# Kernel optimization log

Hardware: AMD Instinct MI355X
Metric: run time of the kernel (lower is better)

The kernel has to match this reference:

```python
import jax, jax.numpy as jnp
import numpy as np

B, S, H, HKV, D = 2, 1024, 32, 8, 128


def _rope_tables(seq_len, head_dim, base=10000.0):
    inv_freq = 1.0 / (base ** (np.arange(0, head_dim, 2, dtype=np.float32) / head_dim))
    freqs = np.arange(seq_len, dtype=np.float32)[:, None] * inv_freq[None, :]  # [S, D/2]
    emb = np.concatenate([freqs, freqs], axis=-1)  # [S, D] (Llama layout)
    return jnp.asarray(np.cos(emb)), jnp.asarray(np.sin(emb))


def setup_inputs() -> dict:
    key = jax.random.key(0)
    kq, kk, kv = jax.random.split(key, 3)
    q = jax.random.normal(kq, (B, S, H, D), dtype=jnp.float32)
    k = jax.random.normal(kk, (B, S, HKV, D), dtype=jnp.float32)
    v = jax.random.normal(kv, (B, S, HKV, D), dtype=jnp.float32)
    cos, sin = _rope_tables(S, D)
    # additive causal mask [B, 1, S, S]: 0 where allowed, large negative where masked
    causal = jnp.tril(jnp.ones((S, S), dtype=bool))
    mask = jnp.where(causal, 0.0, -1e9).astype(jnp.float32)
    attention_mask = jnp.broadcast_to(mask[None, None], (B, 1, S, S))
    softmax_scale = 1.0 / float(np.sqrt(D))
    return {
        "query_states": q, "key_states": k, "value_states": v,
        "cos": cos, "sin": sin, "attention_mask": attention_mask,
        "softmax_scale": softmax_scale,
    }


def _apply_rope(x, cos, sin):
    # x: [B, S, h, D]; cos/sin: [S, D]
    d2 = x.shape[-1] // 2
    rot = jnp.concatenate([-x[..., d2:], x[..., :d2]], axis=-1)  # rotate_half
    return x * cos[None, :, None, :] + rot * sin[None, :, None, :]


def reference(query_states, key_states, value_states, cos, sin, attention_mask, softmax_scale):
    b, s, h, d = query_states.shape
    hkv = key_states.shape[2]
    g = h // hkv  # GQA group size
    q = _apply_rope(query_states, cos, sin)
    k = _apply_rope(key_states, cos, sin)
    qg = q.reshape(b, s, hkv, g, d)
    # scores: [B, Hkv, G, Q, K]
    scores = jnp.einsum('bqhgd,bkhd->bhgqk', qg, k) * softmax_scale
    scores = scores + attention_mask[:, :, None]  # [B,1,Q,K] -> broadcast over (Hkv, G)
    p = jax.nn.softmax(scores, axis=-1)
    out = jnp.einsum('bhgqk,bkhd->bqhgd', p, value_states)
    return out.reshape(b, s, h, d)
```

## Files before the change

kernel.cpp:

```cpp
#include <hip/hip_runtime.h>

#define S_LEN 1024
#define D_DIM 128
#define NH    32
#define NKV   8
#define NB    2

typedef __bf16 bf16x8 __attribute__((ext_vector_type(8)));
typedef float  f32x4  __attribute__((ext_vector_type(4)));
typedef unsigned short u16x8 __attribute__((ext_vector_type(8)));

__device__ __forceinline__ unsigned short f2bf(float f) {
    unsigned int u = __float_as_uint(f);
    u += 0x7fffu + ((u >> 16) & 1u);
    return (unsigned short)(u >> 16);
}

__device__ __forceinline__ void gld_lds16(const unsigned short* g, unsigned short* l) {
    __builtin_amdgcn_global_load_lds(
        (const __attribute__((address_space(1))) unsigned int*)(g),
        (__attribute__((address_space(3))) unsigned int*)(l), 16, 0, 0);
}

__global__ __launch_bounds__(256) void rope_q_kernel(
    const float* __restrict__ q, const float* __restrict__ cosb,
    const float* __restrict__ sinb, const float* __restrict__ scale_ptr,
    unsigned short* __restrict__ Qr)
{
    const float sc = *scale_ptr * 1.44269504088896f;
    int gid = blockIdx.x * 256 + threadIdx.x;
    int row = gid >> 6;
    int j   = gid & 63;
    int h  = row & (NH - 1);
    int bs = row >> 5;
    int s  = bs & (S_LEN - 1);
    int b  = bs >> 10;
    const float* qp = q + (size_t)row * D_DIM;
    float x0 = qp[j];
    float x1 = qp[j + 64];
    float c  = cosb[s * D_DIM + j];
    float sn = sinb[s * D_DIM + j];
    size_t orow = ((size_t)(b * NH + h) * S_LEN + s) * D_DIM;
    Qr[orow + j]      = f2bf((x0 * c - x1 * sn) * sc);
    Qr[orow + j + 64] = f2bf((x1 * c + x0 * sn) * sc);
}

__global__ __launch_bounds__(256) void rope_k_kernel(
    const float* __restrict__ k, const float* __restrict__ cosb,
    const float* __restrict__ sinb, unsigned short* __restrict__ Kr)
{
    int gid = blockIdx.x * 256 + threadIdx.x;
    int row = gid >> 6;
    int j   = gid & 63;
    int hk = row & (NKV - 1);
    int bs = row >> 3;
    int s  = bs & (S_LEN - 1);
    int b  = bs >> 10;
    const float* kp = k + (size_t)row * D_DIM;
    float x0 = kp[j];
    float x1 = kp[j + 64];
    float c  = cosb[s * D_DIM + j];
    float sn = sinb[s * D_DIM + j];
    size_t orow = ((size_t)(b * NKV + hk) * S_LEN + s) * D_DIM;
    Kr[orow + j]      = f2bf(x0 * c - x1 * sn);
    Kr[orow + j + 64] = f2bf(x1 * c + x0 * sn);
}

__global__ __launch_bounds__(256) void transpose_v_kernel(
    const float* __restrict__ v, unsigned short* __restrict__ Vt)
{
    int blk   = blockIdx.x;
    int stile = blk & 15;
    int hk    = (blk >> 4) & (NKV - 1);
    int b     = blk >> 7;
    int tid   = threadIdx.x;
    __shared__ unsigned short tile[64][132];
#pragma unroll
    for (int i = 0; i < 8; i++) {
        int e    = i * 256 + tid;
        int srow = e >> 5;
        int dq   = (e & 31) * 4;
        const float* vp = v + (((size_t)(b * S_LEN + stile * 64 + srow) * NKV + hk) * D_DIM + dq);
        float4 val = *(const float4*)vp;
        tile[srow][dq + 0] = f2bf(val.x);
        tile[srow][dq + 1] = f2bf(val.y);
        tile[srow][dq + 2] = f2bf(val.z);
        tile[srow][dq + 3] = f2bf(val.w);
    }
    __syncthreads();
    size_t head = (size_t)(b * NKV + hk) * D_DIM * S_LEN;
#pragma unroll
    for (int i = 0; i < 4; i++) {
        int g  = i * 256 + tid;
        int d  = g >> 3;
        int c8 = g & 7;
        int s0 = c8 * 8;
        u16x8 pk;
#pragma unroll
        for (int jj = 0; jj < 8; jj++) pk[jj] = tile[s0 + jj][d];
        *(u16x8*)(Vt + head + (size_t)d * S_LEN + stile * 64 + s0) = pk;
    }
}

__global__ __launch_bounds__(256, 2) void attn_kernel(
    const unsigned short* __restrict__ Qr,
    const unsigned short* __restrict__ Kr,
    const unsigned short* __restrict__ Vt,
    float* __restrict__ out)
{
    const int p    = blockIdx.x;
    const int h    = blockIdx.y;
    const int b    = blockIdx.z;
    const int hk   = h >> 2;
    const int tid  = threadIdx.x;
    const int w    = tid >> 6;
    const int lane = tid & 63;
    const int lr   = lane & 15;
    const int lg   = lane >> 4;

    __shared__ unsigned short Kt[2][64 * 128];
    __shared__ unsigned short Vs[2][128 * 64];
    __shared__ unsigned short Pb[4][16 * 64];

    const unsigned short* khead = Kr + (size_t)(b * NKV + hk) * S_LEN * D_DIM;
    const unsigned short* vhead = Vt + (size_t)(b * NKV + hk) * D_DIM * S_LEN;

    auto stage = [&](int u, int buf) {
        const unsigned short* kt = khead + (size_t)u * 64 * D_DIM;
#pragma unroll
        for (int n = 0; n < 4; n++) {
            int row = w * 16 + n * 4 + (lane >> 4);
            int cc  = (lane & 15) ^ (row & 7);
            gld_lds16(kt + (size_t)row * D_DIM + cc * 8,
                      &Kt[buf][(w * 16 + n * 4) * 128]);
        }
        const unsigned short* vt = vhead + u * 64;
#pragma unroll
        for (int n = 0; n < 4; n++) {
            int d  = w * 32 + n * 8 + (lane >> 3);
            int cc = (lane & 7) ^ (d & 7);
            gld_lds16(vt + (size_t)d * S_LEN + cc * 8,
                      &Vs[buf][(w * 32 + n * 8) * 64]);
        }
    };

#pragma unroll 1
    for (int pass = 0; pass < 2; ++pass) {
        const int qt = (pass == 0) ? (15 - p) : p;

        const unsigned short* qbase =
            Qr + ((size_t)(b * NH + h) * S_LEN + qt * 64 + w * 16 + lr) * D_DIM;
        bf16x8 qf[4];
#pragma unroll
        for (int kk = 0; kk < 4; kk++)
            qf[kk] = *(const bf16x8*)(qbase + lg * 8 + kk * 32);

        f32x4 o[8];
#pragma unroll
        for (int dt = 0; dt < 8; dt++) o[dt] = f32x4{0.f, 0.f, 0.f, 0.f};
        float m_run = -1e30f, lsum = 0.f;

        if (pass) __syncthreads();
        stage(0, 0);

#pragma unroll 1
        for (int u = 0; u <= qt; ++u) {
            const int cur = u & 1;
            __syncthreads();
            if (u < qt) stage(u + 1, cur ^ 1);

            f32x4 st[4];
#pragma unroll
            for (int kj = 0; kj < 4; kj++) st[kj] = f32x4{0.f, 0.f, 0.f, 0.f};
            __builtin_amdgcn_s_setprio(1);
#pragma unroll
            for (int kj = 0; kj < 4; kj++) {
                if (u < qt || kj <= w) {
                    int row = kj * 16 + lr;
#pragma unroll
                    for (int kk = 0; kk < 4; kk++) {
                        int cs = (lg + kk * 4) ^ (row & 7);
                        bf16x8 kf = *(const bf16x8*)(&Kt[cur][row * 128 + cs * 8]);
                        st[kj] = __builtin_amdgcn_mfma_f32_16x16x32_bf16(kf, qf[kk], st[kj], 0, 0, 0);
                    }
                }
            }
            __builtin_amdgcn_s_setprio(0);

            if (u == qt) {
#pragma unroll
                for (int kj = 0; kj < 4; kj++)
#pragma unroll
                    for (int r = 0; r < 4; r++)
                        if (kj * 16 + lg * 4 + r > w * 16 + lr) st[kj][r] = -1e30f;
            }

            float lmax = fmaxf(fmaxf(fmaxf(st[0][0], st[0][1]), fmaxf(st[0][2], st[0][3])),
                               fmaxf(fmaxf(st[1][0], st[1][1]), fmaxf(st[1][2], st[1][3])));
            lmax = fmaxf(lmax,
                   fmaxf(fmaxf(fmaxf(st[2][0], st[2][1]), fmaxf(st[2][2], st[2][3])),
                         fmaxf(fmaxf(st[3][0], st[3][1]), fmaxf(st[3][2], st[3][3]))));
            float pm = fmaxf(lmax, __shfl_xor(lmax, 16));
            pm = fmaxf(pm, __shfl_xor(pm, 32));

            if (__any(pm > m_run + 8.f)) {
                float mnew = fmaxf(m_run, pm);
                float ps   = exp2f(m_run - mnew);
                m_run = mnew;
                lsum *= ps;
#pragma unroll
                for (int r = 0; r < 4; r++) {
                    float psr = __shfl(ps, lg * 4 + r);
#pragma unroll
                    for (int dt = 0; dt < 8; dt++) o[dt][r] *= psr;
                }
            }
            float lsloc = 0.f;
#pragma unroll
            for (int kj = 0; kj < 4; kj++)
#pragma unroll
                for (int r = 0; r < 4; r++) {
                    float pv = exp2f(st[kj][r] - m_run);
                    st[kj][r] = pv;
                    lsloc += pv;
                }
            float t = lsloc + __shfl_xor(lsloc, 16);
            t += __shfl_xor(t, 32);
            lsum += t;

            char* pw = (char*)&Pb[w][0];
#pragma unroll
            for (int kj = 0; kj < 4; kj++) {
                unsigned int w0 = (unsigned)f2bf(st[kj][0]) | ((unsigned)f2bf(st[kj][1]) << 16);
                unsigned int w1 = (unsigned)f2bf(st[kj][2]) | ((unsigned)f2bf(st[kj][3]) << 16);
                int C = (2 * kj + (lg >> 1)) ^ (lr & 7);
                *(uint2*)(pw + lr * 128 + C * 16 + (lg & 1) * 8) = uint2{w0, w1};
            }

            __builtin_amdgcn_s_setprio(1);
#pragma unroll
            for (int kk2 = 0; kk2 < 2; kk2++) {
                int Cp = (lg + 4 * kk2) ^ (lr & 7);
                bf16x8 pf = *(const bf16x8*)(pw + lr * 128 + Cp * 16);
#pragma unroll
                for (int dt = 0; dt < 8; dt++) {
                    int vrow = dt * 16 + lr;
                    int cs = (lg + kk2 * 4) ^ (vrow & 7);
                    bf16x8 vf = *(const bf16x8*)(&Vs[cur][vrow * 64 + cs * 8]);
                    o[dt] = __builtin_amdgcn_mfma_f32_16x16x32_bf16(pf, vf, o[dt], 0, 0, 0);
                }
            }
            __builtin_amdgcn_s_setprio(0);
        }

        float rcp = 1.0f / lsum;
        float invr[4];
#pragma unroll
        for (int r = 0; r < 4; r++) invr[r] = __shfl(rcp, lg * 4 + r);
        float* obase = out + ((size_t)(b * S_LEN + qt * 64 + w * 16) * NH + h) * D_DIM;
#pragma unroll
        for (int dt = 0; dt < 8; dt++)
#pragma unroll
            for (int r = 0; r < 4; r++)
                obase[(size_t)(lg * 4 + r) * NH * D_DIM + dt * 16 + lr] = o[dt][r] * invr[r];
    }
}

extern "C" void kernel_launch(void* const* d_in, const int* in_sizes, int n_in,
                              void* d_out, int out_size, void* d_ws, size_t ws_size,
                              hipStream_t stream) {
    const float* q    = (const float*)d_in[0];
    const float* k    = (const float*)d_in[1];
    const float* v    = (const float*)d_in[2];
    const float* cosb = (const float*)d_in[3];
    const float* sinb = (const float*)d_in[4];
    const float* scale = (const float*)d_in[6];
    float* out = (float*)d_out;

    unsigned short* Qr = (unsigned short*)d_ws;
    unsigned short* Kr = Qr + (size_t)NB * NH  * S_LEN * D_DIM;
    unsigned short* Vt = Kr + (size_t)NB * NKV * S_LEN * D_DIM;

    rope_q_kernel<<<NB * S_LEN * NH / 4, 256, 0, stream>>>(q, cosb, sinb, scale, Qr);
    rope_k_kernel<<<NB * S_LEN * NKV / 4, 256, 0, stream>>>(k, cosb, sinb, Kr);
    transpose_v_kernel<<<NB * NKV * (S_LEN / 64), 256, 0, stream>>>(v, Vt);
    dim3 grid(8, NH, NB);
    attn_kernel<<<grid, 256, 0, stream>>>(Qr, Kr, Vt, out);
}
```

Baseline: 66.26 us.

## Switch attention to 32x32x16 MFMA with 512-thread blocks over 256-query tiles

Rewrites the attention kernel to use 32x32x16 bf16 MFMA instructions, with each of 8 waves owning 32 query rows in a 256-row tile. The P matrix stays in registers as the A operand instead of round-tripping through LDS. The paired-tile causal balancing is replaced by a swizzled 1-D grid of 256 blocks. Each K/V tile staged in LDS now serves 256 query rows, which cuts redundant loads, but the causal work is unevenly spread across blocks and waves that sit idle on masked tiles still wait at the barriers.

```diff
diff --git a/kernel.cpp b/kernel.cpp
--- a/kernel.cpp
+++ b/kernel.cpp
@@ -7,8 +7,9 @@
 #define NB    2
 
 typedef __bf16 bf16x8 __attribute__((ext_vector_type(8)));
-typedef float  f32x4  __attribute__((ext_vector_type(4)));
+typedef float  f32x16 __attribute__((ext_vector_type(16)));
 typedef unsigned short u16x8 __attribute__((ext_vector_type(8)));
+typedef unsigned int   u32x4 __attribute__((ext_vector_type(4)));
 
 __device__ __forceinline__ unsigned short f2bf(float f) {
     unsigned int u = __float_as_uint(f);
@@ -74,7 +75,7 @@
     int hk    = (blk >> 4) & (NKV - 1);
     int b     = blk >> 7;
     int tid   = threadIdx.x;
-    __shared__ unsigned short tile[64][132];
+    __shared__ __align__(16) unsigned short tile[64][132];
 #pragma unroll
     for (int i = 0; i < 8; i++) {
         int e    = i * 256 + tid;
@@ -102,106 +103,118 @@
     }
 }
 
-__global__ __launch_bounds__(256, 2) void attn_kernel(
+__global__ __launch_bounds__(512, 2) void attn_kernel(
     const unsigned short* __restrict__ Qr,
     const unsigned short* __restrict__ Kr,
     const unsigned short* __restrict__ Vt,
     float* __restrict__ out)
 {
-    const int p    = blockIdx.x;
-    const int h    = blockIdx.y;
-    const int b    = blockIdx.z;
-    const int hk   = h >> 2;
+    const int bid = blockIdx.x;
+    const int swz = (bid & 7) * 32 + (bid >> 3);
+    const int t  = swz & 3;
+    const int h  = (swz >> 2) & 31;
+    const int b  = swz >> 7;
+    const int hk = h >> 2;
+
     const int tid  = threadIdx.x;
     const int w    = tid >> 6;
     const int lane = tid & 63;
-    const int lr   = lane & 15;
-    const int lg   = lane >> 4;
-
-    __shared__ unsigned short Kt[2][64 * 128];
-    __shared__ unsigned short Vs[2][128 * 64];
-    __shared__ unsigned short Pb[4][16 * 64];
+    const int ln   = lane & 31;
+    const int hi   = lane >> 5;
+
+    __shared__ __align__(16) unsigned short Kt[2][64 * 128];
+    __shared__ __align__(16) unsigned short Vs[2][128 * 64];
+
+    const int q0 = t * 256 + w * 32;
+    const int qg = q0 + ln;
 
     const unsigned short* khead = Kr + (size_t)(b * NKV + hk) * S_LEN * D_DIM;
     const unsigned short* vhead = Vt + (size_t)(b * NKV + hk) * D_DIM * S_LEN;
 
+    const int krow = lane >> 4;
+    const int kcc  = lane & 15;
+    const int vrw  = lane >> 3;
+    const int vcc  = lane & 7;
+
     auto stage = [&](int u, int buf) {
         const unsigned short* kt = khead + (size_t)u * 64 * D_DIM;
 #pragma unroll
-        for (int n = 0; n < 4; n++) {
-            int row = w * 16 + n * 4 + (lane >> 4);
-            int cc  = (lane & 15) ^ (row & 7);
-            gld_lds16(kt + (size_t)row * D_DIM + cc * 8,
-                      &Kt[buf][(w * 16 + n * 4) * 128]);
+        for (int n = 0; n < 2; n++) {
+            int row = w * 8 + n * 4 + krow;
+            int cc  = kcc ^ (row & 7);
+            gld_lds16(kt + (size_t)row * D_DIM + cc * 8, &Kt[buf][(w * 8 + n * 4) * 128]);
         }
-        const unsigned short* vt = vhead + u * 64;
-#pragma unroll
-        for (int n = 0; n < 4; n++) {
-            int d  = w * 32 + n * 8 + (lane >> 3);
-            int cc = (lane & 7) ^ (d & 7);
-            gld_lds16(vt + (size_t)d * S_LEN + cc * 8,
-                      &Vs[buf][(w * 32 + n * 8) * 64]);
+        const unsigned short* vt = vhead + (size_t)u * 64;
+#pragma unroll
+        for (int n = 0; n < 2; n++) {
+            int d  = w * 16 + n * 8 + vrw;
+            int cc = vcc ^ (d & 7);
+            gld_lds16(vt + (size_t)d * S_LEN + cc * 8, &Vs[buf][(w * 16 + n * 8) * 64]);
         }
     };
 
+    const unsigned short* qrow =
+        Qr + ((size_t)(b * NH + h) * S_LEN + qg) * D_DIM + hi * 8;
+    bf16x8 qf[8];
+#pragma unroll
+    for (int dd = 0; dd < 8; dd++)
+        qf[dd] = *(const bf16x8*)(qrow + dd * 16);
+
+    f32x16 o[4];
+#pragma unroll
+    for (int dt = 0; dt < 4; dt++)
+#pragma unroll
+        for (int r = 0; r < 16; r++) o[dt][r] = 0.f;
+    float m_run = -1e30f, lsum = 0.f;
+
+    const int U = 4 * t + 4;
+    stage(0, 0);
+
 #pragma unroll 1
-    for (int pass = 0; pass < 2; ++pass) {
-        const int qt = (pass == 0) ? (15 - p) : p;
-
-        const unsigned short* qbase =
-            Qr + ((size_t)(b * NH + h) * S_LEN + qt * 64 + w * 16 + lr) * D_DIM;
-        bf16x8 qf[4];
-#pragma unroll
-        for (int kk = 0; kk < 4; kk++)
-            qf[kk] = *(const bf16x8*)(qbase + lg * 8 + kk * 32);
-
-        f32x4 o[8];
-#pragma unroll
-        for (int dt = 0; dt < 8; dt++) o[dt] = f32x4{0.f, 0.f, 0.f, 0.f};
-        float m_run = -1e30f, lsum = 0.f;
-
-        if (pass) __syncthreads();
-        stage(0, 0);
-
-#pragma unroll 1
-        for (int u = 0; u <= qt; ++u) {
-            const int cur = u & 1;
-            __syncthreads();
-            if (u < qt) stage(u + 1, cur ^ 1);
-
-            f32x4 st[4];
-#pragma unroll
-            for (int kj = 0; kj < 4; kj++) st[kj] = f32x4{0.f, 0.f, 0.f, 0.f};
+    for (int u = 0; u < U; ++u) {
+        const int cur = u & 1;
+        __syncthreads();
+        if (u + 1 < U) stage(u + 1, cur ^ 1);
+
+        if (64 * u <= q0 + 31) {
+            const bool act1 = (64 * u + 32 <= q0 + 31);
+
+            f32x16 st[2];
+#pragma unroll
+            for (int r = 0; r < 16; r++) { st[0][r] = 0.f; st[1][r] = 0.f; }
             __builtin_amdgcn_s_setprio(1);
 #pragma unroll
-            for (int kj = 0; kj < 4; kj++) {
-                if (u < qt || kj <= w) {
-                    int row = kj * 16 + lr;
-#pragma unroll
-                    for (int kk = 0; kk < 4; kk++) {
-                        int cs = (lg + kk * 4) ^ (row & 7);
-                        bf16x8 kf = *(const bf16x8*)(&Kt[cur][row * 128 + cs * 8]);
-                        st[kj] = __builtin_amdgcn_mfma_f32_16x16x32_bf16(kf, qf[kk], st[kj], 0, 0, 0);
+            for (int s = 0; s < 2; s++) {
+                if (s == 0 || act1) {
+#pragma unroll
+                    for (int dd = 0; dd < 8; dd++) {
+                        int row = s * 32 + ln;
+                        int c   = (2 * dd + hi) ^ (row & 7);
+                        bf16x8 kf = *(const bf16x8*)(&Kt[cur][row * 128 + c * 8]);
+                        st[s] = __builtin_amdgcn_mfma_f32_32x32x16_bf16(kf, qf[dd], st[s], 0, 0, 0);
                     }
                 }
             }
             __builtin_amdgcn_s_setprio(0);
 
-            if (u == qt) {
-#pragma unroll
-                for (int kj = 0; kj < 4; kj++)
-#pragma unroll
-                    for (int r = 0; r < 4; r++)
-                        if (kj * 16 + lg * 4 + r > w * 16 + lr) st[kj][r] = -1e30f;
-            }
-
-            float lmax = fmaxf(fmaxf(fmaxf(st[0][0], st[0][1]), fmaxf(st[0][2], st[0][3])),
-                               fmaxf(fmaxf(st[1][0], st[1][1]), fmaxf(st[1][2], st[1][3])));
-            lmax = fmaxf(lmax,
-                   fmaxf(fmaxf(fmaxf(st[2][0], st[2][1]), fmaxf(st[2][2], st[2][3])),
-                         fmaxf(fmaxf(st[3][0], st[3][1]), fmaxf(st[3][2], st[3][3]))));
-            float pm = fmaxf(lmax, __shfl_xor(lmax, 16));
-            pm = fmaxf(pm, __shfl_xor(pm, 32));
+            if (64 * u + 63 > q0) {
+#pragma unroll
+                for (int s = 0; s < 2; s++)
+#pragma unroll
+                    for (int r = 0; r < 16; r++) {
+                        int kg = 64 * u + 32 * s + (r & 3) + 8 * (r >> 2) + 4 * hi;
+                        if (kg > qg) st[s][r] = -1e30f;
+                    }
+            }
+
+            float mx = -1e30f;
+#pragma unroll
+            for (int r = 0; r < 16; r++) mx = fmaxf(mx, st[0][r]);
+            if (act1) {
+#pragma unroll
+                for (int r = 0; r < 16; r++) mx = fmaxf(mx, st[1][r]);
+            }
+            float pm = fmaxf(mx, __shfl_xor(mx, 32));
 
             if (__any(pm > m_run + 8.f)) {
                 float mnew = fmaxf(m_run, pm);
@@ -209,60 +222,66 @@
                 m_run = mnew;
                 lsum *= ps;
 #pragma unroll
-                for (int r = 0; r < 4; r++) {
-                    float psr = __shfl(ps, lg * 4 + r);
-#pragma unroll
-                    for (int dt = 0; dt < 8; dt++) o[dt][r] *= psr;
+                for (int r = 0; r < 16; r++) {
+                    float psr = __shfl(ps, (r & 3) + 8 * (r >> 2) + 4 * hi);
+#pragma unroll
+                    for (int dt = 0; dt < 4; dt++) o[dt][r] *= psr;
                 }
             }
-            float lsloc = 0.f;
-#pragma unroll
-            for (int kj = 0; kj < 4; kj++)
-#pragma unroll
-                for (int r = 0; r < 4; r++) {
-                    float pv = exp2f(st[kj][r] - m_run);
-                    st[kj][r] = pv;
-                    lsloc += pv;
+            float ls = 0.f;
+#pragma unroll
+            for (int r = 0; r < 16; r++) {
+                float p = exp2f(st[0][r] - m_run);
+                st[0][r] = p; ls += p;
+            }
+            if (act1) {
+#pragma unroll
+                for (int r = 0; r < 16; r++) {
+                    float p = exp2f(st[1][r] - m_run);
+                    st[1][r] = p; ls += p;
                 }
-            float t = lsloc + __shfl_xor(lsloc, 16);
-            t += __shfl_xor(t, 32);
-            lsum += t;
-
-            char* pw = (char*)&Pb[w][0];
-#pragma unroll
-            for (int kj = 0; kj < 4; kj++) {
-                unsigned int w0 = (unsigned)f2bf(st[kj][0]) | ((unsigned)f2bf(st[kj][1]) << 16);
-                unsigned int w1 = (unsigned)f2bf(st[kj][2]) | ((unsigned)f2bf(st[kj][3]) << 16);
-                int C = (2 * kj + (lg >> 1)) ^ (lr & 7);
-                *(uint2*)(pw + lr * 128 + C * 16 + (lg & 1) * 8) = uint2{w0, w1};
-            }
-
+            }
+            lsum += ls + __shfl_xor(ls, 32);
+
+            const char* vbase = (const char*)&Vs[cur][0];
             __builtin_amdgcn_s_setprio(1);
 #pragma unroll
-            for (int kk2 = 0; kk2 < 2; kk2++) {
-                int Cp = (lg + 4 * kk2) ^ (lr & 7);
-                bf16x8 pf = *(const bf16x8*)(pw + lr * 128 + Cp * 16);
-#pragma unroll
-                for (int dt = 0; dt < 8; dt++) {
-                    int vrow = dt * 16 + lr;
-                    int cs = (lg + kk2 * 4) ^ (vrow & 7);
-                    bf16x8 vf = *(const bf16x8*)(&Vs[cur][vrow * 64 + cs * 8]);
-                    o[dt] = __builtin_amdgcn_mfma_f32_16x16x32_bf16(pf, vf, o[dt], 0, 0, 0);
+            for (int ks = 0; ks < 4; ks++) {
+                if (ks < 2 || act1) {
+                    const f32x16& sv = st[ks >> 1];
+                    const int g = (ks & 1) * 8;
+                    unsigned int d0 = (unsigned)f2bf(sv[g + 0]) | ((unsigned)f2bf(sv[g + 1]) << 16);
+                    unsigned int d1 = (unsigned)f2bf(sv[g + 2]) | ((unsigned)f2bf(sv[g + 3]) << 16);
+                    unsigned int d2 = (unsigned)f2bf(sv[g + 4]) | ((unsigned)f2bf(sv[g + 5]) << 16);
+                    unsigned int d3 = (unsigned)f2bf(sv[g + 6]) | ((unsigned)f2bf(sv[g + 7]) << 16);
+                    u32x4 paw = {d0, d1, d2, d3};
+                    bf16x8 pa = __builtin_bit_cast(bf16x8, paw);
+#pragma unroll
+                    for (int dt = 0; dt < 4; dt++) {
+                        int d = dt * 32 + ln;
+                        const char* vrow = vbase + d * 128;
+                        int x = d & 7;
+                        uint2 vlo = *(const uint2*)(vrow + (((2 * ks)     ^ x) * 16) + hi * 8);
+                        uint2 vhi = *(const uint2*)(vrow + (((2 * ks + 1) ^ x) * 16) + hi * 8);
+                        u32x4 vw = {vlo.x, vlo.y, vhi.x, vhi.y};
+                        bf16x8 vf = __builtin_bit_cast(bf16x8, vw);
+                        o[dt] = __builtin_amdgcn_mfma_f32_32x32x16_bf16(pa, vf, o[dt], 0, 0, 0);
+                    }
                 }
             }
             __builtin_amdgcn_s_setprio(0);
         }
-
-        float rcp = 1.0f / lsum;
-        float invr[4];
-#pragma unroll
-        for (int r = 0; r < 4; r++) invr[r] = __shfl(rcp, lg * 4 + r);
-        float* obase = out + ((size_t)(b * S_LEN + qt * 64 + w * 16) * NH + h) * D_DIM;
-#pragma unroll
-        for (int dt = 0; dt < 8; dt++)
-#pragma unroll
-            for (int r = 0; r < 4; r++)
-                obase[(size_t)(lg * 4 + r) * NH * D_DIM + dt * 16 + lr] = o[dt][r] * invr[r];
+    }
+
+    float rcp = 1.0f / lsum;
+    float* ob = out + ((size_t)(b * S_LEN + q0) * NH + h) * D_DIM;
+#pragma unroll
+    for (int r = 0; r < 16; r++) {
+        int qo = (r & 3) + 8 * (r >> 2) + 4 * hi;
+        float invr = __shfl(rcp, qo);
+#pragma unroll
+        for (int dt = 0; dt < 4; dt++)
+            ob[(size_t)qo * NH * D_DIM + dt * 32 + ln] = o[dt][r] * invr;
     }
 }
 
@@ -284,6 +303,5 @@
     rope_q_kernel<<<NB * S_LEN * NH / 4, 256, 0, stream>>>(q, cosb, sinb, scale, Qr);
     rope_k_kernel<<<NB * S_LEN * NKV / 4, 256, 0, stream>>>(k, cosb, sinb, Kr);
     transpose_v_kernel<<<NB * NKV * (S_LEN / 64), 256, 0, stream>>>(v, Vt);
-    dim3 grid(8, NH, NB);
-    attn_kernel<<<grid, 256, 0, stream>>>(Qr, Kr, Vt, out);
-}
+    attn_kernel<<<NB * NH * (S_LEN / 256), 512, 0, stream>>>(Qr, Kr, Vt, out);
+}
```

Measured after the change: 77.05 us. 16.3% more time.

## Merge prep kernels and split attention into one q-tile per block with 32-key tiles

Applied to the files above, without the earlier changes.

The three preprocessing kernels (RoPE on Q, RoPE on K, V transpose) become a single launch that dispatches on block index. The attention kernel drops the two-pass paired q-tile scheme and runs 1024 blocks of one q-tile each, ordered heaviest-first for load balancing. Key/value tiles shrink from 64 to 32, which halves LDS use and lets fully masked 16-row halves be skipped per wave. This removes launch overhead and raises occupancy, but adds twice as many loop iterations and barriers per tile.

```diff
diff --git a/kernel.cpp b/kernel.cpp
--- a/kernel.cpp
+++ b/kernel.cpp
@@ -22,160 +22,166 @@
         (__attribute__((address_space(3))) unsigned int*)(l), 16, 0, 0);
 }
 
-__global__ __launch_bounds__(256) void rope_q_kernel(
-    const float* __restrict__ q, const float* __restrict__ cosb,
+__global__ __launch_bounds__(256) void prep_kernel(
+    const float* __restrict__ q, const float* __restrict__ k,
+    const float* __restrict__ v, const float* __restrict__ cosb,
     const float* __restrict__ sinb, const float* __restrict__ scale_ptr,
-    unsigned short* __restrict__ Qr)
+    unsigned short* __restrict__ Qr, unsigned short* __restrict__ Kr,
+    unsigned short* __restrict__ Vt)
 {
-    const float sc = *scale_ptr * 1.44269504088896f;
-    int gid = blockIdx.x * 256 + threadIdx.x;
-    int row = gid >> 6;
-    int j   = gid & 63;
-    int h  = row & (NH - 1);
-    int bs = row >> 5;
-    int s  = bs & (S_LEN - 1);
-    int b  = bs >> 10;
-    const float* qp = q + (size_t)row * D_DIM;
-    float x0 = qp[j];
-    float x1 = qp[j + 64];
-    float c  = cosb[s * D_DIM + j];
-    float sn = sinb[s * D_DIM + j];
-    size_t orow = ((size_t)(b * NH + h) * S_LEN + s) * D_DIM;
-    Qr[orow + j]      = f2bf((x0 * c - x1 * sn) * sc);
-    Qr[orow + j + 64] = f2bf((x1 * c + x0 * sn) * sc);
-}
-
-__global__ __launch_bounds__(256) void rope_k_kernel(
-    const float* __restrict__ k, const float* __restrict__ cosb,
-    const float* __restrict__ sinb, unsigned short* __restrict__ Kr)
-{
-    int gid = blockIdx.x * 256 + threadIdx.x;
-    int row = gid >> 6;
-    int j   = gid & 63;
-    int hk = row & (NKV - 1);
-    int bs = row >> 3;
-    int s  = bs & (S_LEN - 1);
-    int b  = bs >> 10;
-    const float* kp = k + (size_t)row * D_DIM;
-    float x0 = kp[j];
-    float x1 = kp[j + 64];
-    float c  = cosb[s * D_DIM + j];
-    float sn = sinb[s * D_DIM + j];
-    size_t orow = ((size_t)(b * NKV + hk) * S_LEN + s) * D_DIM;
-    Kr[orow + j]      = f2bf(x0 * c - x1 * sn);
-    Kr[orow + j + 64] = f2bf(x1 * c + x0 * sn);
-}
-
-__global__ __launch_bounds__(256) void transpose_v_kernel(
-    const float* __restrict__ v, unsigned short* __restrict__ Vt)
-{
-    int blk   = blockIdx.x;
-    int stile = blk & 15;
-    int hk    = (blk >> 4) & (NKV - 1);
-    int b     = blk >> 7;
-    int tid   = threadIdx.x;
-    __shared__ unsigned short tile[64][132];
-#pragma unroll
-    for (int i = 0; i < 8; i++) {
-        int e    = i * 256 + tid;
-        int srow = e >> 5;
-        int dq   = (e & 31) * 4;
-        const float* vp = v + (((size_t)(b * S_LEN + stile * 64 + srow) * NKV + hk) * D_DIM + dq);
-        float4 val = *(const float4*)vp;
-        tile[srow][dq + 0] = f2bf(val.x);
-        tile[srow][dq + 1] = f2bf(val.y);
-        tile[srow][dq + 2] = f2bf(val.z);
-        tile[srow][dq + 3] = f2bf(val.w);
+    const int bx  = blockIdx.x;
+    const int tid = threadIdx.x;
+    __shared__ __align__(16) unsigned short tile[64][132];
+    if (bx < 16384) {
+        const float sc = *scale_ptr * 1.44269504088896f;
+        int gid = bx * 256 + tid;
+        int row = gid >> 6;
+        int j   = gid & 63;
+        int h  = row & (NH - 1);
+        int bs = row >> 5;
+        int s  = bs & (S_LEN - 1);
+        int b  = bs >> 10;
+        const float* qp = q + (size_t)row * D_DIM;
+        float x0 = qp[j];
+        float x1 = qp[j + 64];
+        float c  = cosb[s * D_DIM + j];
+        float sn = sinb[s * D_DIM + j];
+        size_t orow = ((size_t)(b * NH + h) * S_LEN + s) * D_DIM;
+        Qr[orow + j]      = f2bf((x0 * c - x1 * sn) * sc);
+        Qr[orow + j + 64] = f2bf((x1 * c + x0 * sn) * sc);
+    } else if (bx < 20480) {
+        int gid = (bx - 16384) * 256 + tid;
+        int row = gid >> 6;
+        int j   = gid & 63;
+        int hk = row & (NKV - 1);
+        int bs = row >> 3;
+        int s  = bs & (S_LEN - 1);
+        int b  = bs >> 10;
+        const float* kp = k + (size_t)row * D_DIM;
+        float x0 = kp[j];
+        float x1 = kp[j + 64];
+        float c  = cosb[s * D_DIM + j];
+        float sn = sinb[s * D_DIM + j];
+        size_t orow = ((size_t)(b * NKV + hk) * S_LEN + s) * D_DIM;
+        Kr[orow + j]      = f2bf(x0 * c - x1 * sn);
+        Kr[orow + j + 64] = f2bf(x1 * c + x0 * sn);
+    } else {
+        int blk   = bx - 20480;
+        int stile = blk & 15;
+        int hk    = (blk >> 4) & (NKV - 1);
+        int b     = blk >> 7;
+#pragma unroll
+        for (int i = 0; i < 8; i++) {
+            int e    = i * 256 + tid;
+            int srow = e >> 5;
+            int dq   = (e & 31) * 4;
+            const float* vp = v + (((size_t)(b * S_LEN + stile * 64 + srow) * NKV + hk) * D_DIM + dq);
+            float4 val = *(const float4*)vp;
+            tile[srow][dq + 0] = f2bf(val.x);
+            tile[srow][dq + 1] = f2bf(val.y);
+            tile[srow][dq + 2] = f2bf(val.z);
+            tile[srow][dq + 3] = f2bf(val.w);
+        }
+        __syncthreads();
+        size_t head = (size_t)(b * NKV + hk) * D_DIM * S_LEN;
+#pragma unroll
+        for (int i = 0; i < 4; i++) {
+            int g  = i * 256 + tid;
+            int d  = g >> 3;
+            int c8 = g & 7;
+            int s0 = c8 * 8;
+            u16x8 pk;
+#pragma unroll
+            for (int jj = 0; jj < 8; jj++) pk[jj] = tile[s0 + jj][d];
+            *(u16x8*)(Vt + head + (size_t)d * S_LEN + stile * 64 + s0) = pk;
+        }
     }
-    __syncthreads();
-    size_t head = (size_t)(b * NKV + hk) * D_DIM * S_LEN;
-#pragma unroll
-    for (int i = 0; i < 4; i++) {
-        int g  = i * 256 + tid;
-        int d  = g >> 3;
-        int c8 = g & 7;
-        int s0 = c8 * 8;
-        u16x8 pk;
-#pragma unroll
-        for (int jj = 0; jj < 8; jj++) pk[jj] = tile[s0 + jj][d];
-        *(u16x8*)(Vt + head + (size_t)d * S_LEN + stile * 64 + s0) = pk;
-    }
-}
-
-__global__ __launch_bounds__(256, 2) void attn_kernel(
+}
+
+__global__ __launch_bounds__(256) void attn_kernel(
     const unsigned short* __restrict__ Qr,
     const unsigned short* __restrict__ Kr,
     const unsigned short* __restrict__ Vt,
     float* __restrict__ out)
 {
-    const int p    = blockIdx.x;
-    const int h    = blockIdx.y;
-    const int b    = blockIdx.z;
+    const int bid = blockIdx.x;
+    const int g   = bid >> 8;
+    const int m   = (bid >> 6) & 3;
+    const int qt  = (g == 0) ? (15 - m) : (g == 1) ? (8 + m)
+                  : (g == 2) ? (7 - m)  : m;
+    const int head = bid & 63;
+    const int h    = head & 31;
+    const int b    = head >> 5;
     const int hk   = h >> 2;
+
     const int tid  = threadIdx.x;
     const int w    = tid >> 6;
     const int lane = tid & 63;
     const int lr   = lane & 15;
     const int lg   = lane >> 4;
 
-    __shared__ unsigned short Kt[2][64 * 128];
-    __shared__ unsigned short Vs[2][128 * 64];
-    __shared__ unsigned short Pb[4][16 * 64];
+    __shared__ __align__(16) unsigned short Kt[2][32 * 128];
+    __shared__ __align__(16) unsigned short Vs[2][128 * 32];
+    __shared__ __align__(16) unsigned short Pb[4][16 * 32];
+
+    const int qw = qt * 64 + w * 16;
+    const int U  = 2 * qt + 2;
 
     const unsigned short* khead = Kr + (size_t)(b * NKV + hk) * S_LEN * D_DIM;
     const unsigned short* vhead = Vt + (size_t)(b * NKV + hk) * D_DIM * S_LEN;
 
+    const int krow = lane >> 4;
+    const int kcc  = lane & 15;
+    const int vrw  = lane >> 2;
+    const int vcc  = lane & 3;
+
     auto stage = [&](int u, int buf) {
-        const unsigned short* kt = khead + (size_t)u * 64 * D_DIM;
-#pragma unroll
-        for (int n = 0; n < 4; n++) {
-            int row = w * 16 + n * 4 + (lane >> 4);
-            int cc  = (lane & 15) ^ (row & 7);
-            gld_lds16(kt + (size_t)row * D_DIM + cc * 8,
-                      &Kt[buf][(w * 16 + n * 4) * 128]);
-        }
-        const unsigned short* vt = vhead + u * 64;
-#pragma unroll
-        for (int n = 0; n < 4; n++) {
-            int d  = w * 32 + n * 8 + (lane >> 3);
-            int cc = (lane & 7) ^ (d & 7);
-            gld_lds16(vt + (size_t)d * S_LEN + cc * 8,
-                      &Vs[buf][(w * 32 + n * 8) * 64]);
+        const unsigned short* kt = khead + (size_t)u * 32 * D_DIM;
+#pragma unroll
+        for (int n = 0; n < 2; n++) {
+            int row = w * 8 + n * 4 + krow;
+            int cc  = kcc ^ (row & 7);
+            gld_lds16(kt + (size_t)row * D_DIM + cc * 8, &Kt[buf][(w * 8 + n * 4) * 128]);
+        }
+        const unsigned short* vt = vhead + (size_t)u * 32;
+#pragma unroll
+        for (int n = 0; n < 2; n++) {
+            int d  = w * 32 + n * 16 + vrw;
+            int cc = vcc ^ (d & 3);
+            gld_lds16(vt + (size_t)d * S_LEN + cc * 8, &Vs[buf][(w * 32 + n * 16) * 32]);
         }
     };
 
+    const unsigned short* qbase =
+        Qr + ((size_t)(b * NH + h) * S_LEN + qw + lr) * D_DIM;
+    bf16x8 qf[4];
+#pragma unroll
+    for (int kk = 0; kk < 4; kk++)
+        qf[kk] = *(const bf16x8*)(qbase + lg * 8 + kk * 32);
+
+    f32x4 o[8];
+#pragma unroll
+    for (int dt = 0; dt < 8; dt++) o[dt] = f32x4{0.f, 0.f, 0.f, 0.f};
+    float m_run = -1e30f, lsum = 0.f;
+
+    stage(0, 0);
+
 #pragma unroll 1
-    for (int pass = 0; pass < 2; ++pass) {
-        const int qt = (pass == 0) ? (15 - p) : p;
-
-        const unsigned short* qbase =
-            Qr + ((size_t)(b * NH + h) * S_LEN + qt * 64 + w * 16 + lr) * D_DIM;
-        bf16x8 qf[4];
-#pragma unroll
-        for (int kk = 0; kk < 4; kk++)
-            qf[kk] = *(const bf16x8*)(qbase + lg * 8 + kk * 32);
-
-        f32x4 o[8];
-#pragma unroll
-        for (int dt = 0; dt < 8; dt++) o[dt] = f32x4{0.f, 0.f, 0.f, 0.f};
-        float m_run = -1e30f, lsum = 0.f;
-
-        if (pass) __syncthreads();
-        stage(0, 0);
-
-#pragma unroll 1
-        for (int u = 0; u <= qt; ++u) {
-            const int cur = u & 1;
-            __syncthreads();
-            if (u < qt) stage(u + 1, cur ^ 1);
-
-            f32x4 st[4];
-#pragma unroll
-            for (int kj = 0; kj < 4; kj++) st[kj] = f32x4{0.f, 0.f, 0.f, 0.f};
+    for (int u = 0; u < U; ++u) {
+        const int cur = u & 1;
+        __syncthreads();
+        if (u + 1 < U) stage(u + 1, cur ^ 1);
+
+        if (32 * u <= qw + 15) {
+            const bool act1 = (32 * u + 16 <= qw + 15);
+
+            f32x4 st[2];
+            st[0] = f32x4{0.f, 0.f, 0.f, 0.f};
+            st[1] = f32x4{0.f, 0.f, 0.f, 0.f};
             __builtin_amdgcn_s_setprio(1);
 #pragma unroll
-            for (int kj = 0; kj < 4; kj++) {
-                if (u < qt || kj <= w) {
+            for (int kj = 0; kj < 2; kj++) {
+                if (kj == 0 || act1) {
                     int row = kj * 16 + lr;
 #pragma unroll
                     for (int kk = 0; kk < 4; kk++) {
@@ -187,20 +193,17 @@
             }
             __builtin_amdgcn_s_setprio(0);
 
-            if (u == qt) {
-#pragma unroll
-                for (int kj = 0; kj < 4; kj++)
+            if (32 * u + 31 > qw) {
+#pragma unroll
+                for (int kj = 0; kj < 2; kj++)
 #pragma unroll
                     for (int r = 0; r < 4; r++)
-                        if (kj * 16 + lg * 4 + r > w * 16 + lr) st[kj][r] = -1e30f;
-            }
-
-            float lmax = fmaxf(fmaxf(fmaxf(st[0][0], st[0][1]), fmaxf(st[0][2], st[0][3])),
-                               fmaxf(fmaxf(st[1][0], st[1][1]), fmaxf(st[1][2], st[1][3])));
-            lmax = fmaxf(lmax,
-                   fmaxf(fmaxf(fmaxf(st[2][0], st[2][1]), fmaxf(st[2][2], st[2][3])),
-                         fmaxf(fmaxf(st[3][0], st[3][1]), fmaxf(st[3][2], st[3][3]))));
-            float pm = fmaxf(lmax, __shfl_xor(lmax, 16));
+                        if (32 * u + kj * 16 + lg * 4 + r > qw + lr) st[kj][r] = -1e30f;
+            }
+
+            float mx = fmaxf(fmaxf(st[0][0], st[0][1]), fmaxf(st[0][2], st[0][3]));
+            mx = fmaxf(mx, fmaxf(fmaxf(st[1][0], st[1][1]), fmaxf(st[1][2], st[1][3])));
+            float pm = fmaxf(mx, __shfl_xor(mx, 16));
             pm = fmaxf(pm, __shfl_xor(pm, 32));
 
             if (__any(pm > m_run + 8.f)) {
@@ -215,55 +218,52 @@
                     for (int dt = 0; dt < 8; dt++) o[dt][r] *= psr;
                 }
             }
-            float lsloc = 0.f;
-#pragma unroll
-            for (int kj = 0; kj < 4; kj++)
+            float ls = 0.f;
+#pragma unroll
+            for (int kj = 0; kj < 2; kj++)
 #pragma unroll
                 for (int r = 0; r < 4; r++) {
-                    float pv = exp2f(st[kj][r] - m_run);
-                    st[kj][r] = pv;
-                    lsloc += pv;
+                    float p = exp2f(st[kj][r] - m_run);
+                    st[kj][r] = p;
+                    ls += p;
                 }
-            float t = lsloc + __shfl_xor(lsloc, 16);
+            float t = ls + __shfl_xor(ls, 16);
             t += __shfl_xor(t, 32);
             lsum += t;
 
             char* pw = (char*)&Pb[w][0];
 #pragma unroll
-            for (int kj = 0; kj < 4; kj++) {
+            for (int kj = 0; kj < 2; kj++) {
                 unsigned int w0 = (unsigned)f2bf(st[kj][0]) | ((unsigned)f2bf(st[kj][1]) << 16);
                 unsigned int w1 = (unsigned)f2bf(st[kj][2]) | ((unsigned)f2bf(st[kj][3]) << 16);
-                int C = (2 * kj + (lg >> 1)) ^ (lr & 7);
-                *(uint2*)(pw + lr * 128 + C * 16 + (lg & 1) * 8) = uint2{w0, w1};
+                int C = (2 * kj + (lg >> 1)) ^ (lr & 3);
+                *(uint2*)(pw + lr * 64 + C * 16 + (lg & 1) * 8) = uint2{w0, w1};
             }
 
             __builtin_amdgcn_s_setprio(1);
-#pragma unroll
-            for (int kk2 = 0; kk2 < 2; kk2++) {
-                int Cp = (lg + 4 * kk2) ^ (lr & 7);
-                bf16x8 pf = *(const bf16x8*)(pw + lr * 128 + Cp * 16);
-#pragma unroll
-                for (int dt = 0; dt < 8; dt++) {
-                    int vrow = dt * 16 + lr;
-                    int cs = (lg + kk2 * 4) ^ (vrow & 7);
-                    bf16x8 vf = *(const bf16x8*)(&Vs[cur][vrow * 64 + cs * 8]);
-                    o[dt] = __builtin_amdgcn_mfma_f32_16x16x32_bf16(pf, vf, o[dt], 0, 0, 0);
-                }
+            int Cp = lg ^ (lr & 3);
+            bf16x8 pf = *(const bf16x8*)(pw + lr * 64 + Cp * 16);
+#pragma unroll
+            for (int dt = 0; dt < 8; dt++) {
+                int vrow = dt * 16 + lr;
+                int cs2 = lg ^ (vrow & 3);
+                bf16x8 vf = *(const bf16x8*)(&Vs[cur][vrow * 32 + cs2 * 8]);
+                o[dt] = __builtin_amdgcn_mfma_f32_16x16x32_bf16(pf, vf, o[dt], 0, 0, 0);
             }
             __builtin_amdgcn_s_setprio(0);
         }
-
-        float rcp = 1.0f / lsum;
-        float invr[4];
-#pragma unroll
-        for (int r = 0; r < 4; r++) invr[r] = __shfl(rcp, lg * 4 + r);
-        float* obase = out + ((size_t)(b * S_LEN + qt * 64 + w * 16) * NH + h) * D_DIM;
-#pragma unroll
-        for (int dt = 0; dt < 8; dt++)
-#pragma unroll
-            for (int r = 0; r < 4; r++)
-                obase[(size_t)(lg * 4 + r) * NH * D_DIM + dt * 16 + lr] = o[dt][r] * invr[r];
     }
+
+    float rcp = 1.0f / lsum;
+    float invr[4];
+#pragma unroll
+    for (int r = 0; r < 4; r++) invr[r] = __shfl(rcp, lg * 4 + r);
+    float* obase = out + ((size_t)(b * S_LEN + qw) * NH + h) * D_DIM;
+#pragma unroll
+    for (int dt = 0; dt < 8; dt++)
+#pragma unroll
+        for (int r = 0; r < 4; r++)
+            obase[(size_t)(lg * 4 + r) * NH * D_DIM + dt * 16 + lr] = o[dt][r] * invr[r];
 }
 
 extern "C" void kernel_launch(void* const* d_in, const int* in_sizes, int n_in,
@@ -281,9 +281,6 @@
     unsigned short* Kr = Qr + (size_t)NB * NH  * S_LEN * D_DIM;
     unsigned short* Vt = Kr + (size_t)NB * NKV * S_LEN * D_DIM;
 
-    rope_q_kernel<<<NB * S_LEN * NH / 4, 256, 0, stream>>>(q, cosb, sinb, scale, Qr);
-    rope_k_kernel<<<NB * S_LEN * NKV / 4, 256, 0, stream>>>(k, cosb, sinb, Kr);
-    transpose_v_kernel<<<NB * NKV * (S_LEN / 64), 256, 0, stream>>>(v, Vt);
-    dim3 grid(8, NH, NB);
-    attn_kernel<<<grid, 256, 0, stream>>>(Qr, Kr, Vt, out);
-}
+    prep_kernel<<<20736, 256, 0, stream>>>(q, k, v, cosb, sinb, scale, Qr, Kr, Vt);
+    attn_kernel<<<1024, 256, 0, stream>>>(Qr, Kr, Vt, out);
+}
```

Result: slower. 73.45 us (+10.9%).
